# Kernel tuning notes

Hardware: AMD Instinct MI355X
Metric: run time of the kernel (lower is better)

The kernel has to match this reference:

```python
import jax, jax.numpy as jnp
import numpy as np
from jax import lax

B, N, T_IN, F_IN = 64, 800, 15, 8
T_OUT = 12
H = 64
NC = 9
KS = [2, 2, 2, 3, 3, 3, 4, 4, 4]
DS = [1, 2, 4, 1, 2, 4, 1, 2, 4]


def setup_inputs() -> dict:
    key = jax.random.key(0)
    ks = jax.random.split(key, 16)
    s = 0.1
    f32 = jnp.float32
    inp = {}
    inp['A'] = jnp.zeros((1,), f32)  # deprecated graph arg, unused
    inp['X'] = jax.random.normal(ks[0], (B, N, T_IN, F_IN), f32)
    # dilated conv weights grouped by kernel size (comps 0-2 k=2, 3-5 k=3, 6-8 k=4)
    inp['convw2'] = jax.random.normal(ks[1], (3, F_IN, F_IN, 2), f32) * s
    inp['convw3'] = jax.random.normal(ks[2], (3, F_IN, F_IN, 3), f32) * s
    inp['convw4'] = jax.random.normal(ks[3], (3, F_IN, F_IN, 4), f32) * s
    inp['convb'] = jax.random.normal(ks[4], (NC, F_IN), f32) * s
    # encoder GRU params (PyTorch layout: W_ih (3H,F), W_hh (3H,H))
    inp['enc_wih'] = jax.random.normal(ks[5], (NC, 3 * H, F_IN), f32) * s
    inp['enc_whh'] = jax.random.normal(ks[6], (NC, 3 * H, H), f32) * s
    inp['enc_bih'] = jax.random.normal(ks[7], (NC, 3 * H), f32) * s
    inp['enc_bhh'] = jax.random.normal(ks[8], (NC, 3 * H), f32) * s
    # decoder GRUCell params (input size 1)
    inp['dec_wih'] = jax.random.normal(ks[9], (NC, 3 * H, 1), f32) * s
    inp['dec_whh'] = jax.random.normal(ks[10], (NC, 3 * H, H), f32) * s
    inp['dec_bih'] = jax.random.normal(ks[11], (NC, 3 * H), f32) * s
    inp['dec_bhh'] = jax.random.normal(ks[12], (NC, 3 * H), f32) * s
    # per-comp readout Linear(H, 1)
    inp['lin_w'] = jax.random.normal(ks[13], (NC, 1, H), f32) * s
    inp['lin_b'] = jax.random.normal(ks[14], (NC, 1), f32) * s
    # node-wise component mixing embedding
    inp['embed'] = jax.random.normal(ks[15], (N, NC), f32)
    return inp


def gru_cell(x, h, wih, whh, bih, bhh):
    # PyTorch GRU semantics
    gi = x @ wih.T + bih  # (B, 3H)
    gh = h @ whh.T + bhh  # (B, 3H)
    ir, iz, in_ = jnp.split(gi, 3, axis=-1)
    hr, hz, hn = jnp.split(gh, 3, axis=-1)
    r = jax.nn.sigmoid(ir + hr)
    z = jax.nn.sigmoid(iz + hz)
    n = jnp.tanh(in_ + r * hn)
    return (1.0 - z) * n + z * h


def reference(A, X, convw2, convw3, convw4, convb, enc_wih, enc_whh, enc_bih,
              enc_bhh, dec_wih, dec_whh, dec_bih, dec_bhh, lin_w, lin_b, embed):
    del A  # deprecated in pure TS model
    Xf = X.reshape(-1, T_IN, F_IN)            # (B*N, T, F)
    xt = jnp.transpose(Xf, (0, 2, 1))         # (B*N, F, T) for conv NCH
    last0 = Xf[:, -1, 0:1]                    # X1[-1, :, 0] -> (B*N, 1)
    BN = Xf.shape[0]
    conv_ws = [convw2[0], convw2[1], convw2[2], convw3[0], convw3[1],
               convw3[2], convw4[0], convw4[1], convw4[2]]
    outs = []
    for r in range(NC):
        # dilated conv over time, VALID padding (length shrinks by d*(k-1))
        h = lax.conv_general_dilated(xt, conv_ws[r], (1,), 'VALID',
                                     rhs_dilation=(DS[r],),
                                     dimension_numbers=('NCH', 'OIH', 'NCH'))
        h = h + convb[r][None, :, None]
        seq = jnp.transpose(h, (2, 0, 1))     # time-major (L, B*N, F)

        ewih, ewhh, ebih, ebhh = enc_wih[r], enc_whh[r], enc_bih[r], enc_bhh[r]

        def enc_step(hc, x_t):
            return gru_cell(x_t, hc, ewih, ewhh, ebih, ebhh), None

        h_enc, _ = lax.scan(enc_step, jnp.zeros((BN, H), X.dtype), seq)

        dwih, dwhh, dbih, dbhh = dec_wih[r], dec_whh[r], dec_bih[r], dec_bhh[r]
        lw, lb = lin_w[r], lin_b[r]

        def dec_step(carry, _):
            hd, lv = carry
            hd = gru_cell(lv, hd, dwih, dwhh, dbih, dbhh)
            v = hd @ lw.T + lb                # (B*N, 1)
            # torch code feeds value.detach() back in
            return (hd, lax.stop_gradient(v)), v[:, 0]

        _, vals = lax.scan(dec_step, (h_enc, last0), None, length=T_OUT)
        outs.append(jnp.transpose(vals).reshape(B, N, T_OUT))  # (B, N, T_out)
    out = jnp.stack(outs, axis=-1)            # (B, N, T_out, NC)
    w = jax.nn.softmax(embed, axis=-1)        # (N, NC)
    return jnp.einsum('bntc,nc->bnt', out, w)
```

## Files before the change

kernel.cpp:

```cpp
#include <hip/hip_runtime.h>
#include <hip/hip_bf16.h>
#include <stdint.h>

typedef unsigned short u16;
typedef unsigned int   u32;
typedef float f32x4  __attribute__((ext_vector_type(4)));
typedef short bf16x8 __attribute__((ext_vector_type(8)));

#define NSEQ 800
#define TOUT 12
#define NC   9
#define LOG2E  1.44269504088896340736f
#define LOG2E2 2.88539008177792681472f

#define WIMG_STRIDE 73728
#define LDS_BHE 0
#define LDS_BXE 24576
#define LDS_BHD 36864
#define LDS_BXD 61440
#define LDS_H   73728
#define LDS_TOTAL 90112
#define BIASE_OFF 663552
#define BIASD_OFF 672768
#define WGT_OFF   681984

__device__ __forceinline__ u16 f2bf(float f){ union{float f;u32 i;}v; v.f=f; u32 x=v.i; return (u16)((x + 0x7fffu + ((x>>16)&1u))>>16); }
__device__ __forceinline__ u32 pkbf(float a, float b){
  union{ __hip_bfloat162 h2; u32 u; } v;
  v.h2 = __float22bfloat162_rn(float2{a,b});
  return v.u;
}

union BXU { uint4 u; bf16x8 v; };

__global__ void prep_kernel(
  const float* __restrict__ cw2, const float* __restrict__ cw3, const float* __restrict__ cw4,
  const float* __restrict__ cbv,
  const float* __restrict__ Ewih, const float* __restrict__ Ewhh,
  const float* __restrict__ Ebih, const float* __restrict__ Ebhh,
  const float* __restrict__ Dwih, const float* __restrict__ Dwhh,
  const float* __restrict__ Dbih, const float* __restrict__ Dbhh,
  const float* __restrict__ emb,
  char* __restrict__ ws)
{
  const int r = blockIdx.x;
  const int tid = threadIdx.x;
  const int K = (r<3) ? 2 : ((r<6) ? 3 : 4);
  char* wimg = ws + (size_t)r*WIMG_STRIDE;

  const float* ewhh = Ewhh + (size_t)r*192*64;
  const float* dwhh = Dwhh + (size_t)r*192*64;
  #pragma unroll 1
  for (int s = tid; s < 1536; s += 512){
    int g = s >> 6, fl = s & 63;
    int ks = g/12, nt = g%12;
    int col = nt*16 + (fl&15);
    float sc = (nt<8) ? LOG2E : LOG2E2;
    u32 we[4] = {0,0,0,0}, wd[4] = {0,0,0,0};
    #pragma unroll
    for (int j=0;j<8;j++){
      int hid = ((j&3)<<4) | (ks*8 + (fl>>4)*2 + (j>>2));
      we[j>>1] |= (u32)f2bf(sc * ewhh[col*64 + hid]) << ((j&1)*16);
      wd[j>>1] |= (u32)f2bf(sc * dwhh[col*64 + hid]) << ((j&1)*16);
    }
    *(uint4*)(wimg + LDS_BHE + s*16) = uint4{we[0],we[1],we[2],we[3]};
    *(uint4*)(wimg + LDS_BHD + s*16) = uint4{wd[0],wd[1],wd[2],wd[3]};
  }
  const float* wih = Ewih + r*192*8;
  const float* cw  = (r<3) ? (cw2 + r*128) : (r<6) ? (cw3 + (r-3)*192) : (cw4 + (r-6)*256);
  const float* dwih = Dwih + r*192;
  #pragma unroll 1
  for (int s = tid; s < 768; s += 512){
    int g = s >> 6, fl = s & 63;
    int col = g*16 + (fl&15);
    int tap = fl>>4;
    float sc = (g<8) ? LOG2E : LOG2E2;
    u32 w[4] = {0,0,0,0};
    if (tap < K){
      #pragma unroll
      for (int j=0;j<8;j++){
        float a = 0.f;
        #pragma unroll
        for (int o=0;o<8;o++) a += wih[col*8+o]*cw[(o*8+j)*K + tap];
        w[j>>1] |= (u32)f2bf(sc*a) << ((j&1)*16);
      }
    }
    *(uint4*)(wimg + LDS_BXE + s*16) = uint4{w[0],w[1],w[2],w[3]};
    u32 w0 = (tap==0) ? (u32)f2bf(sc*dwih[col]) : 0u;
    *(uint4*)(wimg + LDS_BXD + s*16) = uint4{w0,0,0,0};
  }
  if (tid < 16){
    int n = tid;
    const float* bi = Ebih + r*192; const float* bh2 = Ebhh + r*192;
    const float* cb = cbv + r*8;
    float* be = (float*)(ws + BIASE_OFF) + ((size_t)r*16 + n)*16;
    #pragma unroll
    for (int ht=0; ht<4; ht++){
      int hid = ht*16 + n;
      float cR=0.f,cZ=0.f,cN=0.f;
      #pragma unroll
      for (int o=0;o<8;o++){
        cR += wih[hid*8+o]*cb[o];
        cZ += wih[(64+hid)*8+o]*cb[o];
        cN += wih[(128+hid)*8+o]*cb[o];
      }
      be[ht]    = LOG2E  * (bi[hid]     + bh2[hid]     + cR);
      be[4+ht]  = LOG2E  * (bi[64+hid]  + bh2[64+hid]  + cZ);
      be[8+ht]  = LOG2E2 * (bi[128+hid]                + cN);
      be[12+ht] = LOG2E2 *                bh2[128+hid];
    }
  } else if (tid < 32){
    int n = tid - 16;
    const float* bi = Dbih + r*192; const float* bh2 = Dbhh + r*192;
    float* bd = (float*)(ws + BIASD_OFF) + ((size_t)r*16 + n)*16;
    #pragma unroll
    for (int ht=0; ht<4; ht++){
      int hid = ht*16 + n;
      bd[ht]    = LOG2E  * (bi[hid]     + bh2[hid]);
      bd[4+ht]  = LOG2E  * (bi[64+hid]  + bh2[64+hid]);
      bd[8+ht]  = LOG2E2 *  bi[128+hid];
      bd[12+ht] = LOG2E2 *  bh2[128+hid];
    }
  }
  if (r == 0){
    float* wg = (float*)(ws + WGT_OFF);
    #pragma unroll 1
    for (int nb = tid; nb < NSEQ; nb += 512){
      float e[NC], mx = -1e30f;
      #pragma unroll
      for (int c=0;c<NC;c++){ e[c] = emb[nb*NC+c]; mx = fmaxf(mx, e[c]); }
      float sm = 0.f;
      #pragma unroll
      for (int c=0;c<NC;c++){ e[c] = __expf(e[c]-mx); sm += e[c]; }
      float inv = 1.f/sm;
      #pragma unroll
      for (int c=0;c<NC;c++) wg[nb*NC+c] = e[c]*inv;
    }
  }
}

__global__ __launch_bounds__(512, 2) void rnn_kernel(
  const float* __restrict__ X,
  const float* __restrict__ Lw, const float* __restrict__ Lb,
  const char* __restrict__ ws,
  float* __restrict__ out)
{
  __shared__ char LDSC[LDS_TOTAL];
  const int tid = threadIdx.x;
  const int wv  = tid >> 6;
  const int l   = tid & 63;
  const int q   = l >> 4;
  const int n   = l & 15;
  const int r   = blockIdx.y;
  const int seqb = blockIdx.x*128 + wv*16;

  const int Kc[NC]={2,2,2,3,3,3,4,4,4};
  const int Dc[NC]={1,2,4,1,2,4,1,2,4};
  const int K = Kc[r], D = Dc[r];
  const int L = 15 - (K-1)*D;

  const int HB = LDS_H + wv*2048;
  *(uint4*)(LDSC + HB + l*32)      = uint4{0,0,0,0};
  *(uint4*)(LDSC + HB + l*32 + 16) = uint4{0,0,0,0};

  {
    const uint4* src = (const uint4*)(ws + (size_t)r*WIMG_STRIDE);
    #pragma unroll 1
    for (int it=0; it<9; it++){
      int idx = it*512 + tid;
      *(uint4*)(LDSC + idx*16) = src[idx];
    }
  }

  float bR4[4], bZ4[4], bNi4[4], bNh4[4];
  {
    const float* be = (const float*)(ws + BIASE_OFF) + ((size_t)r*16 + n)*16;
    float4 v0 = *(const float4*)(be);
    float4 v1 = *(const float4*)(be+4);
    float4 v2 = *(const float4*)(be+8);
    float4 v3 = *(const float4*)(be+12);
    bR4[0]=v0.x; bR4[1]=v0.y; bR4[2]=v0.z; bR4[3]=v0.w;
    bZ4[0]=v1.x; bZ4[1]=v1.y; bZ4[2]=v1.z; bZ4[3]=v1.w;
    bNi4[0]=v2.x; bNi4[1]=v2.y; bNi4[2]=v2.z; bNi4[3]=v2.w;
    bNh4[0]=v3.x; bNh4[1]=v3.y; bNh4[2]=v3.z; bNh4[3]=v3.w;
  }

  float hO[4][4];
  #pragma unroll
  for (int ht=0;ht<4;ht++) for (int i=0;i<4;i++) hO[ht][i]=0.f;

  const int ra0 = HB + n*128 + (((  q + n)&7)<<4);
  const int ra1 = HB + n*128 + (((4+q + n)&7)<<4);
  int wa[4];
  #pragma unroll
  for (int i=0;i<4;i++){
    int seq = q*4+i;
    wa[i] = HB + seq*128 + ((((n>>1) + seq)&7)<<4) + ((n&1)<<3);
  }

  auto step_core = [&](int bho, int bxo, bf16x8 ax){
    bf16x8 a0 = *(const bf16x8*)(LDSC + ra0);
    bf16x8 a1 = *(const bf16x8*)(LDSC + ra1);
    float hsv[4]; u32 pk01[4], pk23[4];
    #pragma unroll
    for (int ht=0; ht<4; ht++){
      bf16x8 bR0 = *(const bf16x8*)(LDSC + bho + ((      ht)*64 + l)*16);
      bf16x8 bR1 = *(const bf16x8*)(LDSC + bho + ((12  + ht)*64 + l)*16);
      bf16x8 bZ0 = *(const bf16x8*)(LDSC + bho + (( 4 + ht)*64 + l)*16);
      bf16x8 bZ1 = *(const bf16x8*)(LDSC + bho + ((16  + ht)*64 + l)*16);
      bf16x8 bN0 = *(const bf16x8*)(LDSC + bho + (( 8 + ht)*64 + l)*16);
      bf16x8 bN1 = *(const bf16x8*)(LDSC + bho + ((20  + ht)*64 + l)*16);
      bf16x8 xR  = *(const bf16x8*)(LDSC + bxo + ((      ht)*64 + l)*16);
      bf16x8 xZ  = *(const bf16x8*)(LDSC + bxo + (( 4 + ht)*64 + l)*16);
      bf16x8 xN  = *(const bf16x8*)(LDSC + bxo + (( 8 + ht)*64 + l)*16);
      f32x4 aR  = f32x4{bR4[ht],bR4[ht],bR4[ht],bR4[ht]};
      f32x4 aZ  = f32x4{bZ4[ht],bZ4[ht],bZ4[ht],bZ4[ht]};
      f32x4 aNi = f32x4{bNi4[ht],bNi4[ht],bNi4[ht],bNi4[ht]};
      f32x4 aNh = f32x4{bNh4[ht],bNh4[ht],bNh4[ht],bNh4[ht]};
      aR = __builtin_amdgcn_mfma_f32_16x16x32_bf16(a0, bR0, aR,0,0,0);
      aR = __builtin_amdgcn_mfma_f32_16x16x32_bf16(a1, bR1, aR,0,0,0);
      aR = __builtin_amdgcn_mfma_f32_16x16x32_bf16(ax, xR,  aR,0,0,0);
      aZ = __builtin_amdgcn_mfma_f32_16x16x32_bf16(a0, bZ0, aZ,0,0,0);
      aZ = __builtin_amdgcn_mfma_f32_16x16x32_bf16(a1, bZ1, aZ,0,0,0);
      aZ = __builtin_amdgcn_mfma_f32_16x16x32_bf16(ax, xZ,  aZ,0,0,0);
      aNh= __builtin_amdgcn_mfma_f32_16x16x32_bf16(a0, bN0, aNh,0,0,0);
      aNh= __builtin_amdgcn_mfma_f32_16x16x32_bf16(a1, bN1, aNh,0,0,0);
      aNi= __builtin_amdgcn_mfma_f32_16x16x32_bf16(ax, xN,  aNi,0,0,0);
      #pragma unroll
      for (int i=0;i<4;i++){
        float rr = __builtin_amdgcn_rcpf(1.f + __builtin_amdgcn_exp2f(-aR[i]));
        float zz = __builtin_amdgcn_rcpf(1.f + __builtin_amdgcn_exp2f(-aZ[i]));
        float y  = aNi[i] + rr*aNh[i];
        float nn = 1.f - 2.f*__builtin_amdgcn_rcpf(__builtin_amdgcn_exp2f(y) + 1.f);
        float hn = nn + zz*(hO[ht][i]-nn);
        hO[ht][i] = hn;
        if (ht==0)      hsv[i] = hn;
        else if (ht==1) pk01[i] = pkbf(hsv[i], hn);
        else if (ht==2) hsv[i] = hn;
        else            pk23[i] = pkbf(hsv[i], hn);
      }
    }
    #pragma unroll
    for (int i=0;i<4;i++){
      uint2 wv2; wv2.x = pk01[i]; wv2.y = pk23[i];
      *(uint2*)(LDSC + wa[i]) = wv2;
    }
  };

  const float* xb = X + (size_t)(seqb + n)*120 + ((q<K)? q:0)*D*8;
  float4 c0 = *(const float4*)(xb);
  float4 c1 = *(const float4*)(xb + 4);
  __syncthreads();
  #pragma unroll 1
  for (int t=0; t<L; t++){
    int tn = (t+1 < L) ? (t+1) : t;
    float4 n0 = *(const float4*)(xb + tn*8);
    float4 n1 = *(const float4*)(xb + tn*8 + 4);
    BXU a;
    a.u.x = __builtin_amdgcn_perm(__float_as_uint(c0.y), __float_as_uint(c0.x), 0x07060302u);
    a.u.y = __builtin_amdgcn_perm(__float_as_uint(c0.w), __float_as_uint(c0.z), 0x07060302u);
    a.u.z = __builtin_amdgcn_perm(__float_as_uint(c1.y), __float_as_uint(c1.x), 0x07060302u);
    a.u.w = __builtin_amdgcn_perm(__float_as_uint(c1.w), __float_as_uint(c1.z), 0x07060302u);
    step_core(LDS_BHE, LDS_BXE, a.v);
    c0 = n0; c1 = n1;
  }

  {
    const float* bd = (const float*)(ws + BIASD_OFF) + ((size_t)r*16 + n)*16;
    float4 v0 = *(const float4*)(bd);
    float4 v1 = *(const float4*)(bd+4);
    float4 v2 = *(const float4*)(bd+8);
    float4 v3 = *(const float4*)(bd+12);
    bR4[0]=v0.x; bR4[1]=v0.y; bR4[2]=v0.z; bR4[3]=v0.w;
    bZ4[0]=v1.x; bZ4[1]=v1.y; bZ4[2]=v1.z; bZ4[3]=v1.w;
    bNi4[0]=v2.x; bNi4[1]=v2.y; bNi4[2]=v2.z; bNi4[3]=v2.w;
    bNh4[0]=v3.x; bNh4[1]=v3.y; bNh4[2]=v3.z; bNh4[3]=v3.w;
  }
  float lwr[4];
  #pragma unroll
  for (int ht=0; ht<4; ht++) lwr[ht] = Lw[r*64 + ht*16 + n];
  const float lb_ = Lb[r];
  const float wgt = ((const float*)(ws + WGT_OFF))[((seqb + n) % NSEQ)*NC + r];
  float lv = X[(size_t)(seqb + n)*120 + 112];

  #pragma unroll 1
  for (int t=0; t<TOUT; t++){
    BXU a; a.u = uint4{0,0,0,0};
    if (q==0) a.u.x = (u32)f2bf(lv);
    step_core(LDS_BHD, LDS_BXD, a.v);
    float p[4];
    #pragma unroll
    for (int i=0;i<4;i++)
      p[i] = hO[0][i]*lwr[0] + hO[1][i]*lwr[1] + hO[2][i]*lwr[2] + hO[3][i]*lwr[3];
    #pragma unroll
    for (int m=1; m<16; m<<=1){
      #pragma unroll
      for (int i=0;i<4;i++) p[i] += __shfl_xor(p[i], m, 64);
    }
    float s0 = (n&2) ? p[2] : p[0];
    float s1 = (n&2) ? p[3] : p[1];
    float se = (n&1) ? s1 : s0;
    float v = __shfl(se, (n>>2)*16 + (n&3), 64) + lb_;
    lv = v;
    if (q==0) atomicAdd(out + (size_t)(seqb+n)*TOUT + t, wgt*v);
  }
}

extern "C" void kernel_launch(void* const* d_in, const int* in_sizes, int n_in,
                              void* d_out, int out_size, void* d_ws, size_t ws_size,
                              hipStream_t stream)
{
  float* out = (float*)d_out;
  hipMemsetAsync(out, 0, (size_t)out_size*sizeof(float), stream);

  prep_kernel<<<dim3(NC), 512, 0, stream>>>(
    (const float*)d_in[2], (const float*)d_in[3], (const float*)d_in[4],
    (const float*)d_in[5],
    (const float*)d_in[6], (const float*)d_in[7], (const float*)d_in[8], (const float*)d_in[9],
    (const float*)d_in[10],(const float*)d_in[11],(const float*)d_in[12],(const float*)d_in[13],
    (const float*)d_in[16],
    (char*)d_ws);

  dim3 g(NSEQ*64/128, NC);
  rnn_kernel<<<g, 512, 0, stream>>>(
    (const float*)d_in[1],
    (const float*)d_in[14], (const float*)d_in[15],
    (const char*)d_ws,
    out);
}
```

Before: 757.7 us.

## Drop decoder input MFMA, fold scalar input into accumulators, fuse GRU sigmoid/tanh

```diff
diff --git a/kernel.cpp b/kernel.cpp
--- a/kernel.cpp
+++ b/kernel.cpp
@@ -17,9 +17,8 @@
 #define LDS_BHE 0
 #define LDS_BXE 24576
 #define LDS_BHD 36864
-#define LDS_BXD 61440
-#define LDS_H   73728
-#define LDS_TOTAL 90112
+#define LDS_H   61440
+#define LDS_TOTAL 77824
 #define BIASE_OFF 663552
 #define BIASD_OFF 672768
 #define WGT_OFF   681984
@@ -68,7 +67,6 @@
   }
   const float* wih = Ewih + r*192*8;
   const float* cw  = (r<3) ? (cw2 + r*128) : (r<6) ? (cw3 + (r-3)*192) : (cw4 + (r-6)*256);
-  const float* dwih = Dwih + r*192;
   #pragma unroll 1
   for (int s = tid; s < 768; s += 512){
     int g = s >> 6, fl = s & 63;
@@ -86,8 +84,6 @@
       }
     }
     *(uint4*)(wimg + LDS_BXE + s*16) = uint4{w[0],w[1],w[2],w[3]};
-    u32 w0 = (tap==0) ? (u32)f2bf(sc*dwih[col]) : 0u;
-    *(uint4*)(wimg + LDS_BXD + s*16) = uint4{w0,0,0,0};
   }
   if (tid < 16){
     int n = tid;
@@ -141,6 +137,7 @@
 
 __global__ __launch_bounds__(512, 2) void rnn_kernel(
   const float* __restrict__ X,
+  const float* __restrict__ Dwih,
   const float* __restrict__ Lw, const float* __restrict__ Lb,
   const char* __restrict__ ws,
   float* __restrict__ out)
@@ -166,9 +163,9 @@
   {
     const uint4* src = (const uint4*)(ws + (size_t)r*WIMG_STRIDE);
     #pragma unroll 1
-    for (int it=0; it<9; it++){
+    for (int it=0; it<8; it++){
       int idx = it*512 + tid;
-      *(uint4*)(LDSC + idx*16) = src[idx];
+      if (idx < 3840) *(uint4*)(LDSC + idx*16) = src[idx];
     }
   }
 
@@ -198,21 +195,41 @@
     wa[i] = HB + seq*128 + ((((n>>1) + seq)&7)<<4) + ((n&1)<<3);
   }
 
-  auto step_core = [&](int bho, int bxo, bf16x8 ax){
+#define POINTWISE(aR_,aZ_,aNi_,aNh_,HT) \
+    _Pragma("unroll") \
+    for (int i=0;i<4;i++){ \
+      float Er = __builtin_amdgcn_exp2f(-aR_[i]); \
+      float rr = __builtin_amdgcn_rcpf(1.f + Er); \
+      float y  = aNi_[i] + rr*aNh_[i]; \
+      float En = __builtin_amdgcn_exp2f(y); \
+      float Ez = __builtin_amdgcn_exp2f(-aZ_[i]); \
+      float h  = hO[HT][i]; \
+      float e1 = En + 1.f; \
+      float den = e1 + e1*Ez; \
+      float num = En*(Ez+h) + (h-Ez); \
+      float hn = num * __builtin_amdgcn_rcpf(den); \
+      hO[HT][i] = hn; \
+      if (HT==0)      hsv[i] = hn; \
+      else if (HT==1) pk01[i] = pkbf(hsv[i], hn); \
+      else if (HT==2) hsv[i] = hn; \
+      else            pk23[i] = pkbf(hsv[i], hn); \
+    }
+
+  auto step_core = [&](bf16x8 ax){
     bf16x8 a0 = *(const bf16x8*)(LDSC + ra0);
     bf16x8 a1 = *(const bf16x8*)(LDSC + ra1);
     float hsv[4]; u32 pk01[4], pk23[4];
     #pragma unroll
     for (int ht=0; ht<4; ht++){
-      bf16x8 bR0 = *(const bf16x8*)(LDSC + bho + ((      ht)*64 + l)*16);
-      bf16x8 bR1 = *(const bf16x8*)(LDSC + bho + ((12  + ht)*64 + l)*16);
-      bf16x8 bZ0 = *(const bf16x8*)(LDSC + bho + (( 4 + ht)*64 + l)*16);
-      bf16x8 bZ1 = *(const bf16x8*)(LDSC + bho + ((16  + ht)*64 + l)*16);
-      bf16x8 bN0 = *(const bf16x8*)(LDSC + bho + (( 8 + ht)*64 + l)*16);
-      bf16x8 bN1 = *(const bf16x8*)(LDSC + bho + ((20  + ht)*64 + l)*16);
-      bf16x8 xR  = *(const bf16x8*)(LDSC + bxo + ((      ht)*64 + l)*16);
-      bf16x8 xZ  = *(const bf16x8*)(LDSC + bxo + (( 4 + ht)*64 + l)*16);
-      bf16x8 xN  = *(const bf16x8*)(LDSC + bxo + (( 8 + ht)*64 + l)*16);
+      bf16x8 bR0 = *(const bf16x8*)(LDSC + LDS_BHE + ((      ht)*64 + l)*16);
+      bf16x8 bR1 = *(const bf16x8*)(LDSC + LDS_BHE + ((12  + ht)*64 + l)*16);
+      bf16x8 bZ0 = *(const bf16x8*)(LDSC + LDS_BHE + (( 4 + ht)*64 + l)*16);
+      bf16x8 bZ1 = *(const bf16x8*)(LDSC + LDS_BHE + ((16  + ht)*64 + l)*16);
+      bf16x8 bN0 = *(const bf16x8*)(LDSC + LDS_BHE + (( 8 + ht)*64 + l)*16);
+      bf16x8 bN1 = *(const bf16x8*)(LDSC + LDS_BHE + ((20  + ht)*64 + l)*16);
+      bf16x8 xR  = *(const bf16x8*)(LDSC + LDS_BXE + ((      ht)*64 + l)*16);
+      bf16x8 xZ  = *(const bf16x8*)(LDSC + LDS_BXE + (( 4 + ht)*64 + l)*16);
+      bf16x8 xN  = *(const bf16x8*)(LDSC + LDS_BXE + (( 8 + ht)*64 + l)*16);
       f32x4 aR  = f32x4{bR4[ht],bR4[ht],bR4[ht],bR4[ht]};
       f32x4 aZ  = f32x4{bZ4[ht],bZ4[ht],bZ4[ht],bZ4[ht]};
       f32x4 aNi = f32x4{bNi4[ht],bNi4[ht],bNi4[ht],bNi4[ht]};
@@ -226,19 +243,7 @@
       aNh= __builtin_amdgcn_mfma_f32_16x16x32_bf16(a0, bN0, aNh,0,0,0);
       aNh= __builtin_amdgcn_mfma_f32_16x16x32_bf16(a1, bN1, aNh,0,0,0);
       aNi= __builtin_amdgcn_mfma_f32_16x16x32_bf16(ax, xN,  aNi,0,0,0);
-      #pragma unroll
-      for (int i=0;i<4;i++){
-        float rr = __builtin_amdgcn_rcpf(1.f + __builtin_amdgcn_exp2f(-aR[i]));
-        float zz = __builtin_amdgcn_rcpf(1.f + __builtin_amdgcn_exp2f(-aZ[i]));
-        float y  = aNi[i] + rr*aNh[i];
-        float nn = 1.f - 2.f*__builtin_amdgcn_rcpf(__builtin_amdgcn_exp2f(y) + 1.f);
-        float hn = nn + zz*(hO[ht][i]-nn);
-        hO[ht][i] = hn;
-        if (ht==0)      hsv[i] = hn;
-        else if (ht==1) pk01[i] = pkbf(hsv[i], hn);
-        else if (ht==2) hsv[i] = hn;
-        else            pk23[i] = pkbf(hsv[i], hn);
-      }
+      POINTWISE(aR,aZ,aNi,aNh,ht)
     }
     #pragma unroll
     for (int i=0;i<4;i++){
@@ -261,7 +266,7 @@
     a.u.y = __builtin_amdgcn_perm(__float_as_uint(c0.w), __float_as_uint(c0.z), 0x07060302u);
     a.u.z = __builtin_amdgcn_perm(__float_as_uint(c1.y), __float_as_uint(c1.x), 0x07060302u);
     a.u.w = __builtin_amdgcn_perm(__float_as_uint(c1.w), __float_as_uint(c1.z), 0x07060302u);
-    step_core(LDS_BHE, LDS_BXE, a.v);
+    step_core(a.v);
     c0 = n0; c1 = n1;
   }
 
@@ -276,18 +281,62 @@
     bNi4[0]=v2.x; bNi4[1]=v2.y; bNi4[2]=v2.z; bNi4[3]=v2.w;
     bNh4[0]=v3.x; bNh4[1]=v3.y; bNh4[2]=v3.z; bNh4[3]=v3.w;
   }
+  float dwR[4], dwZ[4], dwN[4];
+  {
+    const float* dwih = Dwih + r*192;
+    #pragma unroll
+    for (int ht=0; ht<4; ht++){
+      int hid = ht*16 + n;
+      dwR[ht] = LOG2E  * dwih[hid];
+      dwZ[ht] = LOG2E  * dwih[64+hid];
+      dwN[ht] = LOG2E2 * dwih[128+hid];
+    }
+  }
   float lwr[4];
   #pragma unroll
   for (int ht=0; ht<4; ht++) lwr[ht] = Lw[r*64 + ht*16 + n];
   const float lb_ = Lb[r];
-  const float wgt = ((const float*)(ws + WGT_OFF))[((seqb + n) % NSEQ)*NC + r];
-  float lv = X[(size_t)(seqb + n)*120 + 112];
+  const float wgt = ((const float*)(ws + WGT_OFF))[((seqb + q*4 + (n&3)) % NSEQ)*NC + r];
+  f32x4 lvv;
+  #pragma unroll
+  for (int i=0;i<4;i++) lvv[i] = X[(size_t)(seqb + q*4 + i)*120 + 112];
 
   #pragma unroll 1
   for (int t=0; t<TOUT; t++){
-    BXU a; a.u = uint4{0,0,0,0};
-    if (q==0) a.u.x = (u32)f2bf(lv);
-    step_core(LDS_BHD, LDS_BXD, a.v);
+    {
+      bf16x8 a0 = *(const bf16x8*)(LDSC + ra0);
+      bf16x8 a1 = *(const bf16x8*)(LDSC + ra1);
+      float hsv[4]; u32 pk01[4], pk23[4];
+      #pragma unroll
+      for (int ht=0; ht<4; ht++){
+        bf16x8 bR0 = *(const bf16x8*)(LDSC + LDS_BHD + ((      ht)*64 + l)*16);
+        bf16x8 bR1 = *(const bf16x8*)(LDSC + LDS_BHD + ((12  + ht)*64 + l)*16);
+        bf16x8 bZ0 = *(const bf16x8*)(LDSC + LDS_BHD + (( 4 + ht)*64 + l)*16);
+        bf16x8 bZ1 = *(const bf16x8*)(LDSC + LDS_BHD + ((16  + ht)*64 + l)*16);
+        bf16x8 bN0 = *(const bf16x8*)(LDSC + LDS_BHD + (( 8 + ht)*64 + l)*16);
+        bf16x8 bN1 = *(const bf16x8*)(LDSC + LDS_BHD + ((20  + ht)*64 + l)*16);
+        f32x4 aR, aZ, aNi, aNh;
+        #pragma unroll
+        for (int i=0;i<4;i++){
+          aR[i]  = bR4[ht]  + lvv[i]*dwR[ht];
+          aZ[i]  = bZ4[ht]  + lvv[i]*dwZ[ht];
+          aNi[i] = bNi4[ht] + lvv[i]*dwN[ht];
+          aNh[i] = bNh4[ht];
+        }
+        aR = __builtin_amdgcn_mfma_f32_16x16x32_bf16(a0, bR0, aR,0,0,0);
+        aR = __builtin_amdgcn_mfma_f32_16x16x32_bf16(a1, bR1, aR,0,0,0);
+        aZ = __builtin_amdgcn_mfma_f32_16x16x32_bf16(a0, bZ0, aZ,0,0,0);
+        aZ = __builtin_amdgcn_mfma_f32_16x16x32_bf16(a1, bZ1, aZ,0,0,0);
+        aNh= __builtin_amdgcn_mfma_f32_16x16x32_bf16(a0, bN0, aNh,0,0,0);
+        aNh= __builtin_amdgcn_mfma_f32_16x16x32_bf16(a1, bN1, aNh,0,0,0);
+        POINTWISE(aR,aZ,aNi,aNh,ht)
+      }
+      #pragma unroll
+      for (int i=0;i<4;i++){
+        uint2 wv2; wv2.x = pk01[i]; wv2.y = pk23[i];
+        *(uint2*)(LDSC + wa[i]) = wv2;
+      }
+    }
     float p[4];
     #pragma unroll
     for (int i=0;i<4;i++)
@@ -297,12 +346,12 @@
       #pragma unroll
       for (int i=0;i<4;i++) p[i] += __shfl_xor(p[i], m, 64);
     }
-    float s0 = (n&2) ? p[2] : p[0];
-    float s1 = (n&2) ? p[3] : p[1];
-    float se = (n&1) ? s1 : s0;
-    float v = __shfl(se, (n>>2)*16 + (n&3), 64) + lb_;
-    lv = v;
-    if (q==0) atomicAdd(out + (size_t)(seqb+n)*TOUT + t, wgt*v);
+    #pragma unroll
+    for (int i=0;i<4;i++) lvv[i] = p[i] + lb_;
+    if (n < 4){
+      float vout = (n&2) ? ((n&1)? lvv[3] : lvv[2]) : ((n&1)? lvv[1] : lvv[0]);
+      atomicAdd(out + (size_t)(seqb + q*4 + n)*TOUT + t, wgt*vout);
+    }
   }
 }
 
@@ -324,6 +373,7 @@
   dim3 g(NSEQ*64/128, NC);
   rnn_kernel<<<g, 512, 0, stream>>>(
     (const float*)d_in[1],
+    (const float*)d_in[10],
     (const float*)d_in[14], (const float*)d_in[15],
     (const char*)d_ws,
     out);
```

Result: no change. 745.6 us (-1.6%).
